# Kernel tuning notes

Measured on AMD Instinct MI355X. Metric: run time of the kernel, lower is better.

The kernel has to match this reference:

```python
import jax, jax.numpy as jnp
import numpy as np

NODES = 16384
EDGES = 262144
DIM_A, DIM_V, DIM_D, DIM_L = 64, 32, 16, 8
R0 = 8.0

_e = np.zeros((3, 3, 3), dtype=np.float32)
for _i, _j, _k in ((0, 1, 2), (1, 2, 0), (2, 0, 1)):
    _e[_i, _j, _k] = 1.0
    _e[_i, _k, _j] = -1.0
EPS = jnp.asarray(_e)  # Levi-Civita for the antisymmetric (cross-product) couplings


def radial_encode_edge(r, n, rmax):
    """r: (E, 3) -> (E, n) compactly-supported cosine radial basis."""
    npi = jnp.pi * jnp.arange(n, dtype=r.dtype)
    x_sq = (r * r).sum(-1) / rmax
    return jnp.cos(npi * jnp.sqrt(x_sq)[..., None]) * jax.nn.relu(1.0 - x_sq)[..., None]


def tens_sigmoid_vec(x):
    """Equivariant bounded nonlinearity on order-1 tensors (last axis = 3)."""
    n = jnp.linalg.norm(x, axis=-1, keepdims=True)
    return x * jnp.tanh(n) / jnp.maximum(n, 1e-6)


def setup_inputs() -> dict:
    key = jax.random.key(0)
    ks = jax.random.split(key, 24)
    A, V, D, L = DIM_A, DIM_V, DIM_D, DIM_L
    pshapes = {
        "P_000": (A, L, A), "P_110": (A, L, V), "P_220": (A, L, D),
        "P_011": (V, L, V), "P_101": (V, L, A), "P_121": (V, L, D),
        "P_211": (V, L, V), "P_111": (V, L, V),
        "P_022": (D, L, D), "P_112": (D, L, V), "P_202": (D, L, A),
        "P_222": (D, L, D), "P_212": (D, L, V),
    }
    nfac = (L * max(A, V, D)) ** -0.5
    inp = {
        "x_a": jax.random.normal(ks[0], (NODES, A), jnp.float32),
        "x_v": jax.random.normal(ks[1], (NODES, V, 3), jnp.float32),
        "x_d": jax.random.normal(ks[2], (NODES, D, 3, 3), jnp.float32),
        "r_ij": jax.random.normal(ks[3], (EDGES, 3), jnp.float32),
    }
    for i, (name, shp) in enumerate(pshapes.items()):
        inp[name] = jax.random.normal(ks[4 + i], shp, jnp.float32) * nfac
    inp["src"] = jax.random.randint(ks[20], (EDGES,), 0, NODES)
    inp["dst"] = jax.random.randint(ks[21], (EDGES,), 0, NODES)
    return inp


def _forward(x_a, x_v, x_d, r_ij,
             P_000, P_110, P_220, P_011, P_101, P_121, P_211, P_111,
             P_022, P_112, P_202, P_222, P_212, src, dst):
    n_nodes = x_a.shape[0]
    # per-edge radial basis (left operands, dim_l = 8)
    rad = radial_encode_edge(r_ij, DIM_L, R0)              # (E, L)
    rh = tens_sigmoid_vec(r_ij * (7.0 / R0))               # (E, 3)
    phi_a = rad                                            # (E, L)
    phi_v = rad[..., None] * rh[..., None, :]              # (E, L, 3)
    phi_d = rad[..., None, None] * rh[..., None, None, :] * rh[..., None, :, None]  # (E, L, 3, 3)
    # gather node features at edge sources
    xa, xv, xd = x_a[src], x_v[src], x_d[src]
    # CG-style tensor-product contractions P_{left}{right}{out}
    m_a = (jnp.einsum('clb,el,eb->ec', P_000, phi_a, xa)
           + jnp.einsum('clb,eli,ebi->ec', P_110, phi_v, xv)
           + jnp.einsum('clb,elij,ebij->ec', P_220, phi_d, xd))
    m_v = (jnp.einsum('clb,el,ebi->eci', P_011, phi_a, xv)
           + jnp.einsum('clb,eli,eb->eci', P_101, phi_v, xa)
           + jnp.einsum('clb,elj,ebij->eci', P_121, phi_v, xd)
           + jnp.einsum('clb,elij,ebj->eci', P_211, phi_d, xv)
           + jnp.einsum('ijk,clb,elj,ebk->eci', EPS, P_111, phi_v, xv))
    m_d = (jnp.einsum('clb,el,ebij->ecij', P_022, phi_a, xd)
           + jnp.einsum('clb,eli,ebj->ecij', P_112, phi_v, xv)
           + jnp.einsum('clb,elij,eb->ecij', P_202, phi_d, xa)
           + jnp.einsum('clb,elik,ebkj->ecij', P_222, phi_d, xd)
           + jnp.einsum('jkm,clb,elik,ebm->ecij', EPS, P_212, phi_d, xv))
    # scatter-sum messages to destination nodes
    y_a = jax.ops.segment_sum(m_a, dst, num_segments=n_nodes)
    y_v = jax.ops.segment_sum(m_v, dst, num_segments=n_nodes)
    y_d = jax.ops.segment_sum(m_d, dst, num_segments=n_nodes)
    # pack (a, v, d) channels into one array: (N, A + 3V + 9D)
    return jnp.concatenate([y_a, y_v.reshape(n_nodes, -1), y_d.reshape(n_nodes, -1)], axis=-1)


def reference(x_a, x_v, x_d, r_ij,
              P_000, P_110, P_220, P_011, P_101, P_121, P_211, P_111,
              P_022, P_112, P_202, P_222, P_212, src, dst):
    return _forward(x_a, x_v, x_d, r_ij,
                    P_000, P_110, P_220, P_011, P_101, P_121, P_211, P_111,
                    P_022, P_112, P_202, P_222, P_212, src, dst)
```

## Files before the change

### kernel.cpp

```cpp
#include <hip/hip_runtime.h>

#define NODES    16384
#define EDGES    262144
#define OUT_CH   304
#define EB       16
#define NTHREADS 256

typedef __attribute__((ext_vector_type(8))) short short8;
typedef __attribute__((ext_vector_type(4))) float f32x4;
typedef __attribute__((ext_vector_type(8))) float f32x8;
typedef __attribute__((ext_vector_type(8))) __bf16 bf16x8;
#define MFMA(a,b,c) __builtin_amdgcn_mfma_f32_16x16x32_bf16((a),(b),(c),0,0,0)

#define NB1 100352
#define NB2 36864
#define NB3 2048
#define NPACK (NB1 + NB2 + NB3)

__global__ __launch_bounds__(256) void prep_kernel(
    const float* __restrict__ P000, const float* __restrict__ P110, const float* __restrict__ P220,
    const float* __restrict__ P011, const float* __restrict__ P101, const float* __restrict__ P121,
    const float* __restrict__ P211, const float* __restrict__ P111,
    const float* __restrict__ P022, const float* __restrict__ P112, const float* __restrict__ P202,
    const float* __restrict__ P222, const float* __restrict__ P212,
    unsigned short* __restrict__ BP,
    const int* __restrict__ dst, int* __restrict__ cnt)
{
    int idx = blockIdx.x*256 + threadIdx.x;
    if (idx < NPACK) {
        float v = 0.0f;
        if (idx < NB1) {
            int j = idx & 7, lane = (idx >> 3) & 63, q = idx >> 9;
            int tile = q % 7, kk = q / 7;
            int n = tile*16 + (lane & 15);
            int k = kk*32 + (lane >> 4)*8 + j;
            int l = k / 112, b = k % 112;
            if (n < 64) {           int c = n;
                if      (b <  64) v = P000[(c*8+l)*64 + b];
                else if (b <  96) v = P110[(c*8+l)*32 + (b-64)];
                else              v = P220[(c*8+l)*16 + (b-96)];
            } else if (n < 96) {    int c = n - 64;
                if      (b <  64) v = P101[(c*8+l)*64 + b];
                else if (b <  96) v = P211[(c*8+l)*32 + (b-64)];
            } else {                int c = n - 96;
                if      (b <  64) v = P202[(c*8+l)*64 + b];
            }
        } else if (idx < NB1 + NB2) {
            int o = idx - NB1;
            int j = o & 7, lane = (o >> 3) & 63, q = o >> 9;
            int tile = q % 3, kk = q / 3;
            int n = tile*16 + (lane & 15);
            int k = kk*32 + (lane >> 4)*8 + j;
            int l = k / 96, b = k % 96;
            if (n < 32) {           int c = n;
                if      (b <  32) v = P011[(c*8+l)*32 + b];
                else if (b <  48) v = P121[(c*8+l)*16 + (b-32)];
                else if (b <  80) v = P111[(c*8+l)*32 + (b-48)];
            } else {                int c = n - 32;
                if      (b <  32) v = P112[(c*8+l)*32 + b];
                else if (b <  48) v = 0.0f;
                else if (b <  80) v = P212[(c*8+l)*32 + (b-48)];
                else              v = P222[(c*8+l)*16 + (b-80)];
            }
        } else {
            int o = idx - NB1 - NB2;
            int j = o & 7, lane = (o >> 3) & 63, kk = o >> 9;
            int n = lane & 15;
            int k = kk*32 + (lane >> 4)*8 + j;
            int l = k / 16, b = k % 16;
            v = P022[(n*8+l)*16 + b];
        }
        union { float f; unsigned int i; } x; x.f = v;
        unsigned int i = x.i;
        i += 0x7fffu + ((i >> 16) & 1u);
        BP[idx] = (unsigned short)(i >> 16);
    }
    if (idx < EDGES) atomicAdd(&cnt[dst[idx]], 1);
}

__global__ __launch_bounds__(256) void scan_kernel(const int* __restrict__ cnt,
                                                   int* __restrict__ off,
                                                   int* __restrict__ cursor)
{
    __shared__ int s_part[256];
    const int t = threadIdx.x;
    const int base = t * 64;
    int sum = 0;
    for (int i = 0; i < 64; ++i) sum += cnt[base + i];
    s_part[t] = sum;
    __syncthreads();
    for (int d = 1; d < 256; d <<= 1) {
        int add = (t >= d) ? s_part[t - d] : 0;
        __syncthreads();
        s_part[t] += add;
        __syncthreads();
    }
    int run = s_part[t] - sum;
    for (int i = 0; i < 64; ++i) {
        int c = cnt[base + i];
        off[base + i]    = run;
        cursor[base + i] = run;
        run += c;
    }
    if (t == 255) off[NODES] = run;
}

__global__ __launch_bounds__(256) void scatter_kernel(const int* __restrict__ dst,
                                                      int* __restrict__ cursor,
                                                      int* __restrict__ eidx)
{
    int e = blockIdx.x*256 + threadIdx.x;
    if (e < EDGES) {
        int pos = atomicAdd(&cursor[dst[e]], 1);
        eidx[pos] = e;
    }
}

template<int BW>
__device__ __forceinline__ short8 build_afrag(const float* __restrict__ frow,
                                              const float* __restrict__ radrow,
                                              int kbase)
{
    const int l  = kbase / BW;
    const int b0 = kbase % BW;
    const float r = radrow[l];
    union { float4 q[2]; f32x8 v; } u;
    u.q[0] = *reinterpret_cast<const float4*>(frow + b0);
    u.q[1] = *reinterpret_cast<const float4*>(frow + b0 + 4);
    f32x8 z = u.v * r;
    bf16x8 zb = __builtin_convertvector(z, bf16x8);
    union { bf16x8 b; short8 s; } w; w.b = zb;
    return w.s;
}

struct FeatPool {
    float FS[EB][116];
    float FVT[EB][3][100];
};
union Pool {
    FeatPool f;
    float m[EB][308];
};

__global__ __launch_bounds__(NTHREADS, 3) void edge_kernel(
    const float* __restrict__ xa_g, const float* __restrict__ xv_g, const float* __restrict__ xd_g,
    const float* __restrict__ rij_g,
    const unsigned short* __restrict__ BP,
    const int* __restrict__ src, const int* __restrict__ dst, const int* __restrict__ eidx,
    float* __restrict__ out)
{
    __shared__ __align__(16) Pool s_p;
    __shared__ __align__(16) float s_FDT[EB][9][20];
    __shared__ float s_as0[EB][32];
    __shared__ float s_a00[EB][16];
    __shared__ float s_aj[EB][3][16];
    __shared__ float s_rad[EB][9];
    __shared__ float s_rh[EB][4];
    __shared__ int   s_dst[EB];
    __shared__ int   s_srcn[EB];

    const int t  = threadIdx.x;
    const int e0 = blockIdx.x * EB;
    const int lane = t & 63, wid = t >> 6;
    const int col = lane & 15, quad = lane >> 4;

    const short8* __restrict__ B1 = (const short8*)BP;
    const short8* __restrict__ B2 = (const short8*)(BP + NB1);
    const short8* __restrict__ B3 = (const short8*)(BP + NB1 + NB2);

    if (t < EB) {
        const int e = eidx[e0 + t];
        float r0 = rij_g[e*3+0];
        float r1 = rij_g[e*3+1];
        float r2 = rij_g[e*3+2];
        float x_sq = (r0*r0 + r1*r1 + r2*r2) * 0.125f;
        float q  = sqrtf(x_sq);
        float w  = fmaxf(1.0f - x_sq, 0.0f);
        const float PI = 3.14159265358979323846f;
        for (int n = 0; n < 8; ++n)
            s_rad[t][n] = cosf(PI * (float)n * q) * w;
        float y0 = r0*0.875f, y1 = r1*0.875f, y2 = r2*0.875f;
        float nn = sqrtf(y0*y0 + y1*y1 + y2*y2);
        float sc = tanhf(nn) / fmaxf(nn, 1e-6f);
        s_rh[t][0] = y0*sc; s_rh[t][1] = y1*sc; s_rh[t][2] = y2*sc; s_rh[t][3] = 0.f;
        s_dst[t]  = dst[e];
        s_srcn[t] = src[e];
    }
    __syncthreads();

    {
        const int el  = t >> 4;
        const int sub = t & 15;
        const int n   = s_srcn[el];
        const float rh0 = s_rh[el][0], rh1 = s_rh[el][1], rh2 = s_rh[el][2];
        #pragma unroll
        for (int k = 0; k < 4; ++k) {
            int b = sub + 16*k;
            s_p.f.FS[el][b] = xa_g[n*64 + b];
        }
        #pragma unroll
        for (int k = 0; k < 2; ++k) {
            int b = sub + 16*k;
            float v0 = xv_g[(n*32 + b)*3 + 0];
            float v1 = xv_g[(n*32 + b)*3 + 1];
            float v2 = xv_g[(n*32 + b)*3 + 2];
            s_p.f.FVT[el][0][b] = v0;
            s_p.f.FVT[el][1][b] = v1;
            s_p.f.FVT[el][2][b] = v2;
            s_p.f.FS[el][64 + b] = rh0*v0 + rh1*v1 + rh2*v2;
            s_p.f.FVT[el][0][48 + b] = rh1*v2 - rh2*v1;
            s_p.f.FVT[el][1][48 + b] = rh2*v0 - rh0*v2;
            s_p.f.FVT[el][2][48 + b] = rh0*v1 - rh1*v0;
        }
        {
            const int b = sub;
            const float d0 = xd_g[(n*16+b)*9+0], d1 = xd_g[(n*16+b)*9+1], d2 = xd_g[(n*16+b)*9+2];
            const float d3 = xd_g[(n*16+b)*9+3], d4 = xd_g[(n*16+b)*9+4], d5 = xd_g[(n*16+b)*9+5];
            const float d6 = xd_g[(n*16+b)*9+6], d7 = xd_g[(n*16+b)*9+7], d8 = xd_g[(n*16+b)*9+8];
            s_FDT[el][0][b]=d0; s_FDT[el][1][b]=d1; s_FDT[el][2][b]=d2;
            s_FDT[el][3][b]=d3; s_FDT[el][4][b]=d4; s_FDT[el][5][b]=d5;
            s_FDT[el][6][b]=d6; s_FDT[el][7][b]=d7; s_FDT[el][8][b]=d8;
            const float uv0 = d0*rh0 + d1*rh1 + d2*rh2;
            const float uv1 = d3*rh0 + d4*rh1 + d5*rh2;
            const float uv2 = d6*rh0 + d7*rh1 + d8*rh2;
            s_p.f.FVT[el][0][32 + b] = uv0;
            s_p.f.FVT[el][1][32 + b] = uv1;
            s_p.f.FVT[el][2][32 + b] = uv2;
            s_p.f.FVT[el][0][80 + b] = rh0*d0 + rh1*d3 + rh2*d6;
            s_p.f.FVT[el][1][80 + b] = rh0*d1 + rh1*d4 + rh2*d7;
            s_p.f.FVT[el][2][80 + b] = rh0*d2 + rh1*d5 + rh2*d8;
            s_p.f.FS[el][96 + b] = rh0*uv0 + rh1*uv1 + rh2*uv2;
        }
    }
    __syncthreads();

    const float* __restrict__ radrow = &s_rad[col][0];
    const int r0 = quad*4;
    f32x4 R0={0,0,0,0}, R1={0,0,0,0}, R2={0,0,0,0}, R3={0,0,0,0};
    f32x4 R4={0,0,0,0}, R5={0,0,0,0}, R6={0,0,0,0}, R7={0,0,0,0};

    if (wid == 0) {
        const float* frow = &s_p.f.FS[col][0];
        for (int kk = 0; kk < 28; ++kk) {
            short8 a = build_afrag<112>(frow, radrow, kk*32 + quad*8);
            const short8* bp = B1 + (kk*7)*64 + lane;
            R0 = MFMA(a, bp[0*64], R0);
            R1 = MFMA(a, bp[1*64], R1);
            R2 = MFMA(a, bp[2*64], R2);
            R3 = MFMA(a, bp[3*64], R3);
        }
        {
            const float* fd0 = &s_FDT[col][0][0];
            const float* fd1 = &s_FDT[col][1][0];
            const float* fd2 = &s_FDT[col][2][0];
            const float* fd3 = &s_FDT[col][3][0];
            #pragma unroll
            for (int kk = 0; kk < 4; ++kk) {
                const short8 b3 = B3[kk*64 + lane];
                R4 = MFMA(build_afrag<16>(fd0, radrow, kk*32 + quad*8), b3, R4);
                R5 = MFMA(build_afrag<16>(fd1, radrow, kk*32 + quad*8), b3, R5);
                R6 = MFMA(build_afrag<16>(fd2, radrow, kk*32 + quad*8), b3, R6);
                R7 = MFMA(build_afrag<16>(fd3, radrow, kk*32 + quad*8), b3, R7);
            }
        }
    } else if (wid == 1) {
        const float* frow = &s_p.f.FS[col][0];
        for (int kk = 0; kk < 28; ++kk) {
            short8 a = build_afrag<112>(frow, radrow, kk*32 + quad*8);
            const short8* bp = B1 + (kk*7)*64 + lane;
            R0 = MFMA(a, bp[4*64], R0);
            R1 = MFMA(a, bp[5*64], R1);
            R2 = MFMA(a, bp[6*64], R2);
        }
        {
            const float* fd4 = &s_FDT[col][4][0];
            const float* fd5 = &s_FDT[col][5][0];
            const float* fd6 = &s_FDT[col][6][0];
            const float* fd7 = &s_FDT[col][7][0];
            const float* fd8 = &s_FDT[col][8][0];
            #pragma unroll
            for (int kk = 0; kk < 4; ++kk) {
                const short8 b3 = B3[kk*64 + lane];
                R3 = MFMA(build_afrag<16>(fd4, radrow, kk*32 + quad*8), b3, R3);
                R4 = MFMA(build_afrag<16>(fd5, radrow, kk*32 + quad*8), b3, R4);
                R5 = MFMA(build_afrag<16>(fd6, radrow, kk*32 + quad*8), b3, R5);
                R6 = MFMA(build_afrag<16>(fd7, radrow, kk*32 + quad*8), b3, R6);
                R7 = MFMA(build_afrag<16>(fd8, radrow, kk*32 + quad*8), b3, R7);
            }
        }
    } else if (wid == 2) {
        const float* f0 = &s_p.f.FVT[col][0][0];
        const float* f1 = &s_p.f.FVT[col][1][0];
        for (int kk = 0; kk < 24; ++kk) {
            short8 a0 = build_afrag<96>(f0, radrow, kk*32 + quad*8);
            short8 a1 = build_afrag<96>(f1, radrow, kk*32 + quad*8);
            const short8* bp = B2 + (kk*3)*64 + lane;
            short8 b0 = bp[0*64], b1 = bp[1*64], b2 = bp[2*64];
            R0 = MFMA(a0, b0, R0);
            R1 = MFMA(a0, b1, R1);
            R2 = MFMA(a0, b2, R2);
            R3 = MFMA(a1, b0, R3);
            R4 = MFMA(a1, b1, R4);
        }
    } else {
        const float* f1 = &s_p.f.FVT[col][1][0];
        const float* f2 = &s_p.f.FVT[col][2][0];
        for (int kk = 0; kk < 24; ++kk) {
            short8 a1 = build_afrag<96>(f1, radrow, kk*32 + quad*8);
            short8 a2 = build_afrag<96>(f2, radrow, kk*32 + quad*8);
            const short8* bp = B2 + (kk*3)*64 + lane;
            short8 b0 = bp[0*64], b1 = bp[1*64], b2 = bp[2*64];
            R0 = MFMA(a1, b2, R0);
            R1 = MFMA(a2, b0, R1);
            R2 = MFMA(a2, b1, R2);
            R3 = MFMA(a2, b2, R3);
        }
    }
    __syncthreads();

    if (wid == 0) {
        #pragma unroll
        for (int r = 0; r < 4; ++r) {
            s_p.m[r0+r][ 0+col] = R0[r];
            s_p.m[r0+r][16+col] = R1[r];
            s_p.m[r0+r][32+col] = R2[r];
            s_p.m[r0+r][48+col] = R3[r];
            s_p.m[r0+r][160 + col*9 + 0] = R4[r];
            s_p.m[r0+r][160 + col*9 + 1] = R5[r];
            s_p.m[r0+r][160 + col*9 + 2] = R6[r];
            s_p.m[r0+r][160 + col*9 + 3] = R7[r];
        }
    } else if (wid == 1) {
        #pragma unroll
        for (int r = 0; r < 4; ++r) {
            s_as0[r0+r][ 0+col] = R0[r];
            s_as0[r0+r][16+col] = R1[r];
            s_a00[r0+r][col]    = R2[r];
            s_p.m[r0+r][160 + col*9 + 4] = R3[r];
            s_p.m[r0+r][160 + col*9 + 5] = R4[r];
            s_p.m[r0+r][160 + col*9 + 6] = R5[r];
            s_p.m[r0+r][160 + col*9 + 7] = R6[r];
            s_p.m[r0+r][160 + col*9 + 8] = R7[r];
        }
    } else if (wid == 2) {
        #pragma unroll
        for (int r = 0; r < 4; ++r) {
            s_p.m[r0+r][64 + ( 0+col)*3 + 0] = R0[r];
            s_p.m[r0+r][64 + (16+col)*3 + 0] = R1[r];
            s_aj[r0+r][0][col]               = R2[r];
            s_p.m[r0+r][64 + ( 0+col)*3 + 1] = R3[r];
            s_p.m[r0+r][64 + (16+col)*3 + 1] = R4[r];
        }
    } else {
        #pragma unroll
        for (int r = 0; r < 4; ++r) {
            s_aj[r0+r][1][col]               = R0[r];
            s_p.m[r0+r][64 + ( 0+col)*3 + 2] = R1[r];
            s_p.m[r0+r][64 + (16+col)*3 + 2] = R2[r];
            s_aj[r0+r][2][col]               = R3[r];
        }
    }
    __syncthreads();

    #pragma unroll
    for (int it = t; it < EB*32; it += NTHREADS) {
        const int el = it >> 5, c = it & 31;
        const float as0 = s_as0[el][c];
        s_p.m[el][64 + c*3 + 0] += s_rh[el][0]*as0;
        s_p.m[el][64 + c*3 + 1] += s_rh[el][1]*as0;
        s_p.m[el][64 + c*3 + 2] += s_rh[el][2]*as0;
    }
    {
        const int el = t >> 4, c = t & 15;
        const float a00 = s_a00[el][c];
        const float aj0 = s_aj[el][0][c], aj1 = s_aj[el][1][c], aj2 = s_aj[el][2][c];
        const float rr0 = s_rh[el][0], rr1 = s_rh[el][1], rr2 = s_rh[el][2];
        const float g0 = aj0 + rr0*a00, g1 = aj1 + rr1*a00, g2 = aj2 + rr2*a00;
        float* md = &s_p.m[el][160 + c*9];
        md[0] += rr0*g0; md[1] += rr0*g1; md[2] += rr0*g2;
        md[3] += rr1*g0; md[4] += rr1*g1; md[5] += rr1*g2;
        md[6] += rr2*g0; md[7] += rr2*g1; md[8] += rr2*g2;
    }
    __syncthreads();

    for (int ch = t; ch < OUT_CH; ch += NTHREADS) {
        float run = 0.0f;
        #pragma unroll
        for (int el = 0; el < EB; ++el) {
            run += s_p.m[el][ch];
            if (el == EB-1 || s_dst[el+1] != s_dst[el]) {
                atomicAdd(&out[(size_t)s_dst[el]*OUT_CH + ch], run);
                run = 0.0f;
            }
        }
    }
}

extern "C" void kernel_launch(void* const* d_in, const int* in_sizes, int n_in,
                              void* d_out, int out_size, void* d_ws, size_t ws_size,
                              hipStream_t stream)
{
    const float* xa  = (const float*)d_in[0];
    const float* xv  = (const float*)d_in[1];
    const float* xd  = (const float*)d_in[2];
    const float* rij = (const float*)d_in[3];
    const float* P000 = (const float*)d_in[4];
    const float* P110 = (const float*)d_in[5];
    const float* P220 = (const float*)d_in[6];
    const float* P011 = (const float*)d_in[7];
    const float* P101 = (const float*)d_in[8];
    const float* P121 = (const float*)d_in[9];
    const float* P211 = (const float*)d_in[10];
    const float* P111 = (const float*)d_in[11];
    const float* P022 = (const float*)d_in[12];
    const float* P112 = (const float*)d_in[13];
    const float* P202 = (const float*)d_in[14];
    const float* P222 = (const float*)d_in[15];
    const float* P212 = (const float*)d_in[16];
    const int* src = (const int*)d_in[17];
    const int* dst = (const int*)d_in[18];

    unsigned short* BP = (unsigned short*)d_ws;
    int* ip     = (int*)d_ws + (NPACK/2);
    int* cnt    = ip;
    int* off    = ip + NODES;
    int* cursor = off + NODES + 1;
    int* eidx   = cursor + NODES;

    hipMemsetAsync(cnt, 0, NODES * sizeof(int), stream);
    hipMemsetAsync(d_out, 0, (size_t)out_size * sizeof(float), stream);

    prep_kernel<<<EDGES/256, 256, 0, stream>>>(
        P000, P110, P220, P011, P101, P121, P211, P111,
        P022, P112, P202, P222, P212, BP, dst, cnt);
    scan_kernel   <<<1,         256, 0, stream>>>(cnt, off, cursor);
    scatter_kernel<<<EDGES/256, 256, 0, stream>>>(dst, cursor, eidx);

    edge_kernel<<<EDGES/EB, NTHREADS, 0, stream>>>(
        xa, xv, xd, rij, BP, src, dst, eidx, (float*)d_out);
}
```

Baseline: 447.0 us.

## Reorder GEMM K dimension to l-fastest and build A fragments from radial vector

```diff
diff --git a/kernel.cpp b/kernel.cpp
--- a/kernel.cpp
+++ b/kernel.cpp
@@ -34,7 +34,7 @@
             int tile = q % 7, kk = q / 7;
             int n = tile*16 + (lane & 15);
             int k = kk*32 + (lane >> 4)*8 + j;
-            int l = k / 112, b = k % 112;
+            int l = k & 7, b = k >> 3;
             if (n < 64) {           int c = n;
                 if      (b <  64) v = P000[(c*8+l)*64 + b];
                 else if (b <  96) v = P110[(c*8+l)*32 + (b-64)];
@@ -51,7 +51,7 @@
             int tile = q % 3, kk = q / 3;
             int n = tile*16 + (lane & 15);
             int k = kk*32 + (lane >> 4)*8 + j;
-            int l = k / 96, b = k % 96;
+            int l = k & 7, b = k >> 3;
             if (n < 32) {           int c = n;
                 if      (b <  32) v = P011[(c*8+l)*32 + b];
                 else if (b <  48) v = P121[(c*8+l)*16 + (b-32)];
@@ -67,7 +67,7 @@
             int j = o & 7, lane = (o >> 3) & 63, kk = o >> 9;
             int n = lane & 15;
             int k = kk*32 + (lane >> 4)*8 + j;
-            int l = k / 16, b = k % 16;
+            int l = k & 7, b = k >> 3;
             v = P022[(n*8+l)*16 + b];
         }
         union { float f; unsigned int i; } x; x.f = v;
@@ -116,18 +116,9 @@
     }
 }
 
-template<int BW>
-__device__ __forceinline__ short8 build_afrag(const float* __restrict__ frow,
-                                              const float* __restrict__ radrow,
-                                              int kbase)
-{
-    const int l  = kbase / BW;
-    const int b0 = kbase % BW;
-    const float r = radrow[l];
-    union { float4 q[2]; f32x8 v; } u;
-    u.q[0] = *reinterpret_cast<const float4*>(frow + b0);
-    u.q[1] = *reinterpret_cast<const float4*>(frow + b0 + 4);
-    f32x8 z = u.v * r;
+__device__ __forceinline__ short8 build2(const f32x8 radv, float f)
+{
+    f32x8 z = radv * f;
     bf16x8 zb = __builtin_convertvector(z, bf16x8);
     union { bf16x8 b; short8 s; } w; w.b = zb;
     return w.s;
@@ -137,12 +128,18 @@
     float FS[EB][116];
     float FVT[EB][3][100];
 };
+struct MsgPool {
+    float m[EB][308];
+    float as0[EB][32];
+    float a00[EB][16];
+    float aj[EB][3][16];
+};
 union Pool {
     FeatPool f;
-    float m[EB][308];
+    MsgPool  g;
 };
 
-__global__ __launch_bounds__(NTHREADS, 3) void edge_kernel(
+__global__ __launch_bounds__(NTHREADS, 4) void edge_kernel(
     const float* __restrict__ xa_g, const float* __restrict__ xv_g, const float* __restrict__ xd_g,
     const float* __restrict__ rij_g,
     const unsigned short* __restrict__ BP,
@@ -151,9 +148,6 @@
 {
     __shared__ __align__(16) Pool s_p;
     __shared__ __align__(16) float s_FDT[EB][9][20];
-    __shared__ float s_as0[EB][32];
-    __shared__ float s_a00[EB][16];
-    __shared__ float s_aj[EB][3][16];
     __shared__ float s_rad[EB][9];
     __shared__ float s_rh[EB][4];
     __shared__ int   s_dst[EB];
@@ -234,7 +228,9 @@
     }
     __syncthreads();
 
-    const float* __restrict__ radrow = &s_rad[col][0];
+    f32x8 radv;
+    #pragma unroll
+    for (int l = 0; l < 8; ++l) radv[l] = s_rad[col][l];
     const int r0 = quad*4;
     f32x4 R0={0,0,0,0}, R1={0,0,0,0}, R2={0,0,0,0}, R3={0,0,0,0};
     f32x4 R4={0,0,0,0}, R5={0,0,0,0}, R6={0,0,0,0}, R7={0,0,0,0};
@@ -242,58 +238,48 @@
     if (wid == 0) {
         const float* frow = &s_p.f.FS[col][0];
         for (int kk = 0; kk < 28; ++kk) {
-            short8 a = build_afrag<112>(frow, radrow, kk*32 + quad*8);
+            short8 a = build2(radv, frow[kk*4 + quad]);
             const short8* bp = B1 + (kk*7)*64 + lane;
             R0 = MFMA(a, bp[0*64], R0);
             R1 = MFMA(a, bp[1*64], R1);
             R2 = MFMA(a, bp[2*64], R2);
             R3 = MFMA(a, bp[3*64], R3);
         }
-        {
-            const float* fd0 = &s_FDT[col][0][0];
-            const float* fd1 = &s_FDT[col][1][0];
-            const float* fd2 = &s_FDT[col][2][0];
-            const float* fd3 = &s_FDT[col][3][0];
-            #pragma unroll
-            for (int kk = 0; kk < 4; ++kk) {
-                const short8 b3 = B3[kk*64 + lane];
-                R4 = MFMA(build_afrag<16>(fd0, radrow, kk*32 + quad*8), b3, R4);
-                R5 = MFMA(build_afrag<16>(fd1, radrow, kk*32 + quad*8), b3, R5);
-                R6 = MFMA(build_afrag<16>(fd2, radrow, kk*32 + quad*8), b3, R6);
-                R7 = MFMA(build_afrag<16>(fd3, radrow, kk*32 + quad*8), b3, R7);
-            }
+        #pragma unroll
+        for (int kk = 0; kk < 4; ++kk) {
+            const int kq = kk*4 + quad;
+            const short8 b3 = B3[kk*64 + lane];
+            R4 = MFMA(build2(radv, s_FDT[col][0][kq]), b3, R4);
+            R5 = MFMA(build2(radv, s_FDT[col][1][kq]), b3, R5);
+            R6 = MFMA(build2(radv, s_FDT[col][2][kq]), b3, R6);
+            R7 = MFMA(build2(radv, s_FDT[col][3][kq]), b3, R7);
         }
     } else if (wid == 1) {
         const float* frow = &s_p.f.FS[col][0];
         for (int kk = 0; kk < 28; ++kk) {
-            short8 a = build_afrag<112>(frow, radrow, kk*32 + quad*8);
+            short8 a = build2(radv, frow[kk*4 + quad]);
             const short8* bp = B1 + (kk*7)*64 + lane;
             R0 = MFMA(a, bp[4*64], R0);
             R1 = MFMA(a, bp[5*64], R1);
             R2 = MFMA(a, bp[6*64], R2);
         }
-        {
-            const float* fd4 = &s_FDT[col][4][0];
-            const float* fd5 = &s_FDT[col][5][0];
-            const float* fd6 = &s_FDT[col][6][0];
-            const float* fd7 = &s_FDT[col][7][0];
-            const float* fd8 = &s_FDT[col][8][0];
-            #pragma unroll
-            for (int kk = 0; kk < 4; ++kk) {
-                const short8 b3 = B3[kk*64 + lane];
-                R3 = MFMA(build_afrag<16>(fd4, radrow, kk*32 + quad*8), b3, R3);
-                R4 = MFMA(build_afrag<16>(fd5, radrow, kk*32 + quad*8), b3, R4);
-                R5 = MFMA(build_afrag<16>(fd6, radrow, kk*32 + quad*8), b3, R5);
-                R6 = MFMA(build_afrag<16>(fd7, radrow, kk*32 + quad*8), b3, R6);
-                R7 = MFMA(build_afrag<16>(fd8, radrow, kk*32 + quad*8), b3, R7);
-            }
+        #pragma unroll
+        for (int kk = 0; kk < 4; ++kk) {
+            const int kq = kk*4 + quad;
+            const short8 b3 = B3[kk*64 + lane];
+            R3 = MFMA(build2(radv, s_FDT[col][4][kq]), b3, R3);
+            R4 = MFMA(build2(radv, s_FDT[col][5][kq]), b3, R4);
+            R5 = MFMA(build2(radv, s_FDT[col][6][kq]), b3, R5);
+            R6 = MFMA(build2(radv, s_FDT[col][7][kq]), b3, R6);
+            R7 = MFMA(build2(radv, s_FDT[col][8][kq]), b3, R7);
         }
     } else if (wid == 2) {
         const float* f0 = &s_p.f.FVT[col][0][0];
         const float* f1 = &s_p.f.FVT[col][1][0];
         for (int kk = 0; kk < 24; ++kk) {
-            short8 a0 = build_afrag<96>(f0, radrow, kk*32 + quad*8);
-            short8 a1 = build_afrag<96>(f1, radrow, kk*32 + quad*8);
+            const int kq = kk*4 + quad;
+            short8 a0 = build2(radv, f0[kq]);
+            short8 a1 = build2(radv, f1[kq]);
             const short8* bp = B2 + (kk*3)*64 + lane;
             short8 b0 = bp[0*64], b1 = bp[1*64], b2 = bp[2*64];
             R0 = MFMA(a0, b0, R0);
@@ -306,8 +292,9 @@
         const float* f1 = &s_p.f.FVT[col][1][0];
         const float* f2 = &s_p.f.FVT[col][2][0];
         for (int kk = 0; kk < 24; ++kk) {
-            short8 a1 = build_afrag<96>(f1, radrow, kk*32 + quad*8);
-            short8 a2 = build_afrag<96>(f2, radrow, kk*32 + quad*8);
+            const int kq = kk*4 + quad;
+            short8 a1 = build2(radv, f1[kq]);
+            short8 a2 = build2(radv, f2[kq]);
             const short8* bp = B2 + (kk*3)*64 + lane;
             short8 b0 = bp[0*64], b1 = bp[1*64], b2 = bp[2*64];
             R0 = MFMA(a1, b2, R0);
@@ -321,43 +308,43 @@
     if (wid == 0) {
         #pragma unroll
         for (int r = 0; r < 4; ++r) {
-            s_p.m[r0+r][ 0+col] = R0[r];
-            s_p.m[r0+r][16+col] = R1[r];
-            s_p.m[r0+r][32+col] = R2[r];
-            s_p.m[r0+r][48+col] = R3[r];
-            s_p.m[r0+r][160 + col*9 + 0] = R4[r];
-            s_p.m[r0+r][160 + col*9 + 1] = R5[r];
-            s_p.m[r0+r][160 + col*9 + 2] = R6[r];
-            s_p.m[r0+r][160 + col*9 + 3] = R7[r];
+            s_p.g.m[r0+r][ 0+col] = R0[r];
+            s_p.g.m[r0+r][16+col] = R1[r];
+            s_p.g.m[r0+r][32+col] = R2[r];
+            s_p.g.m[r0+r][48+col] = R3[r];
+            s_p.g.m[r0+r][160 + col*9 + 0] = R4[r];
+            s_p.g.m[r0+r][160 + col*9 + 1] = R5[r];
+            s_p.g.m[r0+r][160 + col*9 + 2] = R6[r];
+            s_p.g.m[r0+r][160 + col*9 + 3] = R7[r];
         }
     } else if (wid == 1) {
         #pragma unroll
         for (int r = 0; r < 4; ++r) {
-            s_as0[r0+r][ 0+col] = R0[r];
-            s_as0[r0+r][16+col] = R1[r];
-            s_a00[r0+r][col]    = R2[r];
-            s_p.m[r0+r][160 + col*9 + 4] = R3[r];
-            s_p.m[r0+r][160 + col*9 + 5] = R4[r];
-            s_p.m[r0+r][160 + col*9 + 6] = R5[r];
-            s_p.m[r0+r][160 + col*9 + 7] = R6[r];
-            s_p.m[r0+r][160 + col*9 + 8] = R7[r];
+            s_p.g.as0[r0+r][ 0+col] = R0[r];
+            s_p.g.as0[r0+r][16+col] = R1[r];
+            s_p.g.a00[r0+r][col]    = R2[r];
+            s_p.g.m[r0+r][160 + col*9 + 4] = R3[r];
+            s_p.g.m[r0+r][160 + col*9 + 5] = R4[r];
+            s_p.g.m[r0+r][160 + col*9 + 6] = R5[r];
+            s_p.g.m[r0+r][160 + col*9 + 7] = R6[r];
+            s_p.g.m[r0+r][160 + col*9 + 8] = R7[r];
         }
     } else if (wid == 2) {
         #pragma unroll
         for (int r = 0; r < 4; ++r) {
-            s_p.m[r0+r][64 + ( 0+col)*3 + 0] = R0[r];
-            s_p.m[r0+r][64 + (16+col)*3 + 0] = R1[r];
-            s_aj[r0+r][0][col]               = R2[r];
-            s_p.m[r0+r][64 + ( 0+col)*3 + 1] = R3[r];
-            s_p.m[r0+r][64 + (16+col)*3 + 1] = R4[r];
+            s_p.g.m[r0+r][64 + ( 0+col)*3 + 0] = R0[r];
+            s_p.g.m[r0+r][64 + (16+col)*3 + 0] = R1[r];
+            s_p.g.aj[r0+r][0][col]             = R2[r];
+            s_p.g.m[r0+r][64 + ( 0+col)*3 + 1] = R3[r];
+            s_p.g.m[r0+r][64 + (16+col)*3 + 1] = R4[r];
         }
     } else {
         #pragma unroll
         for (int r = 0; r < 4; ++r) {
-            s_aj[r0+r][1][col]               = R0[r];
-            s_p.m[r0+r][64 + ( 0+col)*3 + 2] = R1[r];
-            s_p.m[r0+r][64 + (16+col)*3 + 2] = R2[r];
-            s_aj[r0+r][2][col]               = R3[r];
+            s_p.g.aj[r0+r][1][col]             = R0[r];
+            s_p.g.m[r0+r][64 + ( 0+col)*3 + 2] = R1[r];
+            s_p.g.m[r0+r][64 + (16+col)*3 + 2] = R2[r];
+            s_p.g.aj[r0+r][2][col]             = R3[r];
         }
     }
     __syncthreads();
@@ -365,18 +352,18 @@
     #pragma unroll
     for (int it = t; it < EB*32; it += NTHREADS) {
         const int el = it >> 5, c = it & 31;
-        const float as0 = s_as0[el][c];
-        s_p.m[el][64 + c*3 + 0] += s_rh[el][0]*as0;
-        s_p.m[el][64 + c*3 + 1] += s_rh[el][1]*as0;
-        s_p.m[el][64 + c*3 + 2] += s_rh[el][2]*as0;
+        const float as0 = s_p.g.as0[el][c];
+        s_p.g.m[el][64 + c*3 + 0] += s_rh[el][0]*as0;
+        s_p.g.m[el][64 + c*3 + 1] += s_rh[el][1]*as0;
+        s_p.g.m[el][64 + c*3 + 2] += s_rh[el][2]*as0;
     }
     {
         const int el = t >> 4, c = t & 15;
-        const float a00 = s_a00[el][c];
-        const float aj0 = s_aj[el][0][c], aj1 = s_aj[el][1][c], aj2 = s_aj[el][2][c];
+        const float a00 = s_p.g.a00[el][c];
+        const float aj0 = s_p.g.aj[el][0][c], aj1 = s_p.g.aj[el][1][c], aj2 = s_p.g.aj[el][2][c];
         const float rr0 = s_rh[el][0], rr1 = s_rh[el][1], rr2 = s_rh[el][2];
         const float g0 = aj0 + rr0*a00, g1 = aj1 + rr1*a00, g2 = aj2 + rr2*a00;
-        float* md = &s_p.m[el][160 + c*9];
+        float* md = &s_p.g.m[el][160 + c*9];
         md[0] += rr0*g0; md[1] += rr0*g1; md[2] += rr0*g2;
         md[3] += rr1*g0; md[4] += rr1*g1; md[5] += rr1*g2;
         md[6] += rr2*g0; md[7] += rr2*g1; md[8] += rr2*g2;
@@ -387,7 +374,7 @@
         float run = 0.0f;
         #pragma unroll
         for (int el = 0; el < EB; ++el) {
-            run += s_p.m[el][ch];
+            run += s_p.g.m[el][ch];
             if (el == EB-1 || s_dst[el+1] != s_dst[el]) {
                 atomicAdd(&out[(size_t)s_dst[el]*OUT_CH + ch], run);
                 run = 0.0f;
```

After: 407.6 us. 8.8% less time.
